# Kernel tuning notes

Hardware: AMD Instinct MI355X
Metric: run time of the kernel (lower is better)

## Reference

```python
import jax, jax.numpy as jnp
import numpy as np
from math import exp

C1 = 0.01 ** 2
C2 = 0.03 ** 2
WINDOW_SIZE = 11
SIGMA = 1.5

def make_window(window_size, channel, sigma=SIGMA):
    g = np.array([exp(-(x - window_size // 2) ** 2 / float(2 * sigma ** 2))
                  for x in range(window_size)], dtype=np.float32)
    g = g / g.sum()
    w2d = np.outer(g, g).astype(np.float32)  # [ws, ws]
    # depthwise kernel, OIHW with I=1 per group: [C, 1, ws, ws]
    return jnp.asarray(np.broadcast_to(w2d, (channel, 1, window_size, window_size)).copy())

def depthwise_conv(x, window, pad):
    C = x.shape[1]
    return jax.lax.conv_general_dilated(
        x, window, window_strides=(1, 1),
        padding=[(pad, pad), (pad, pad)],
        feature_group_count=C,
        dimension_numbers=('NCHW', 'OIHW', 'NCHW'))

def setup_inputs() -> dict:
    key = jax.random.key(0)
    k1, k2 = jax.random.split(key)
    B, C, H, W = 16, 3, 512, 512
    img1 = jax.random.uniform(k1, (B, C, H, W), dtype=jnp.float32)
    img2 = jax.random.uniform(k2, (B, C, H, W), dtype=jnp.float32)
    window = make_window(WINDOW_SIZE, C)
    return {"img1": img1, "img2": img2, "window": window}

def reference(img1, img2, window):
    pad = WINDOW_SIZE // 2
    mu1 = depthwise_conv(img1, window, pad)
    mu2 = depthwise_conv(img2, window, pad)
    mu1_sq = mu1 * mu1
    mu2_sq = mu2 * mu2
    mu1_mu2 = mu1 * mu2
    sigma1_sq = depthwise_conv(img1 * img1, window, pad) - mu1_sq
    sigma2_sq = depthwise_conv(img2 * img2, window, pad) - mu2_sq
    sigma12 = depthwise_conv(img1 * img2, window, pad) - mu1_mu2
    ssim_cs = (2 * sigma12 + C2) / (sigma1_sq + sigma2_sq + C2)
    ssim_l = (2 * mu1_mu2 + C1) / (mu1_sq + mu2_sq + C1)
    ssim_map = ssim_l * ssim_cs
    return jnp.mean(ssim_map)
```

## Files before the change

### kernel.cpp

```cpp
#include <hip/hip_runtime.h>


typedef float v2f __attribute__((ext_vector_type(2)));

#define IMG_H 512
#define IMG_W 512
#define N_IMG 48
#define WS 11
#define PAD 5
#define CHUNK 16
#define NCHUNK (IMG_H / CHUNK)
#define RING 12
#define PLANE_B 5248
#define NPLANE 4
#define INV_NPX (1.0f / (48.0f * 512.0f * 512.0f))

__device__ __forceinline__ unsigned swz8(int E) {
    return (unsigned)((E + (E >> 2)) * 8);
}
__device__ __forceinline__ v2f vfma(v2f a, v2f b, v2f c) {
    return __builtin_elementwise_fma(a, b, c);
}
__device__ __forceinline__ float uni(float x) {
    return __int_as_float(__builtin_amdgcn_readfirstlane(__float_as_int(x)));
}

__global__ __launch_bounds__(256, 5) void ssim_partial_kernel(
    const float* __restrict__ img1,
    const float* __restrict__ img2,
    const float* __restrict__ window,
    float* __restrict__ out)
{
    __shared__ __align__(16) char lds[NPLANE * PLANE_B];
    __shared__ float wred[4];

    const int tid = threadIdx.x;
    const int bc  = blockIdx.x;
    const int r0  = blockIdx.y * CHUNK;
    const int c0  = tid * 2;

    float g[WS];
    {
        const float g5  = sqrtf(window[5 * WS + 5]);
        const float inv = 1.0f / g5;
#pragma unroll
        for (int j = 0; j < WS; ++j) g[j] = uni(window[5 * WS + j] * inv);
    }
    const float C1v = 0.01f * 0.01f;
    const float C2v = 0.03f * 0.03f;

    const float* __restrict__ p1 = img1 + (size_t)bc * (IMG_H * IMG_W);
    const float* __restrict__ p2 = img2 + (size_t)bc * (IMG_H * IMG_W);

    if (tid < 48) {
        const int pj = tid / 12, h = tid % 12;
        const int E  = (h < 6) ? h : (512 + h);
        *(v2f*)(lds + pj * PLANE_B + swz8(E)) = (v2f)(0.0f);
    }
    __syncthreads();

    const unsigned woffA = swz8(c0 + 6);
    const unsigned woffB = swz8(c0 + 7);
    unsigned roff[12];
#pragma unroll
    for (int m = 0; m < 12; ++m) roff[m] = swz8(c0 + 1 + m);

    v2f rx1[RING], rx2[RING];
#pragma unroll
    for (int i = 0; i < RING; ++i) { rx1[i] = (v2f)(0.0f); rx2[i] = (v2f)(0.0f); }

#pragma unroll
    for (int i = 0; i < 10; ++i) {
        const int rr = r0 - PAD + i;
        v2f u1 = (v2f)(0.0f), u2 = (v2f)(0.0f);
        if (rr >= 0 && rr < IMG_H) {
            u1 = *(const v2f*)(p1 + rr * IMG_W + c0);
            u2 = *(const v2f*)(p2 + rr * IMG_W + c0);
        }
        rx1[2 + i] = u1; rx2[2 + i] = u2;
    }
    v2f pend1[2], pend2[2];
#pragma unroll
    for (int j = 0; j < 2; ++j) {
        const int rr = r0 + PAD + j;
        v2f u1 = (v2f)(0.0f), u2 = (v2f)(0.0f);
        if (rr < IMG_H) {
            u1 = *(const v2f*)(p1 + rr * IMG_W + c0);
            u2 = *(const v2f*)(p2 + rr * IMG_W + c0);
        }
        pend1[j] = u1; pend2[j] = u2;
    }

    float acc = 0.0f;

#pragma unroll 1
    for (int step = 0; step < CHUNK / 2; ++step) {
        const int R = r0 + step * 2;

#pragma unroll
        for (int i = 0; i < RING - 2; ++i) { rx1[i] = rx1[i + 2]; rx2[i] = rx2[i + 2]; }
        rx1[10] = pend1[0]; rx2[10] = pend2[0];
        rx1[11] = pend1[1]; rx2[11] = pend2[1];

        if (step + 1 < CHUNK / 2) {
#pragma unroll
            for (int j = 0; j < 2; ++j) {
                const int rr = R + 7 + j;
                v2f u1 = (v2f)(0.0f), u2 = (v2f)(0.0f);
                if (rr < IMG_H) {
                    u1 = *(const v2f*)(p1 + rr * IMG_W + c0);
                    u2 = *(const v2f*)(p2 + rr * IMG_W + c0);
                }
                pend1[j] = u1; pend2[j] = u2;
            }
        }

        v2f va[4][2];
        {
            v2f a0[2] = {(v2f)(0.0f), (v2f)(0.0f)};
            v2f a1[2] = {(v2f)(0.0f), (v2f)(0.0f)};
#pragma unroll
            for (int k = 0; k < 2; ++k)
#pragma unroll
                for (int i = 0; i < WS; ++i) {
                    const v2f w = (v2f)(g[i]);
                    a0[k] = vfma(w, rx1[i + k], a0[k]);
                    a1[k] = vfma(w, rx2[i + k], a1[k]);
                }
            va[0][0] = a0[0]; va[0][1] = a0[1];
            va[1][0] = a1[0]; va[1][1] = a1[1];
        }
        {
            v2f b0[2] = {(v2f)(0.0f), (v2f)(0.0f)};
            v2f b1[2] = {(v2f)(0.0f), (v2f)(0.0f)};
#pragma unroll
            for (int u = 0; u < RING; ++u) {
                const v2f X1 = rx1[u], X2 = rx2[u];
                const v2f S = vfma(X1, X1, X2 * X2);
                const v2f P = X1 * X2;
                if (u <= 10) {
                    b0[0] = vfma((v2f)(g[u]), S, b0[0]);
                    b1[0] = vfma((v2f)(g[u]), P, b1[0]);
                }
                if (u >= 1) {
                    b0[1] = vfma((v2f)(g[u - 1]), S, b0[1]);
                    b1[1] = vfma((v2f)(g[u - 1]), P, b1[1]);
                }
            }
            va[2][0] = b0[0]; va[2][1] = b0[1];
            va[3][0] = b1[0]; va[3][1] = b1[1];
        }
#pragma unroll
        for (int p = 0; p < 4; ++p) {
            char* base = lds + p * PLANE_B;
            *(v2f*)(base + woffA) = (v2f){va[p][0].x, va[p][1].x};
            *(v2f*)(base + woffB) = (v2f){va[p][0].y, va[p][1].y};
        }
        __syncthreads();

        v2f hA[4], hB[4];
#pragma unroll
        for (int p = 0; p < 4; ++p) {
            const char* base = lds + p * PLANE_B;
            v2f r[12];
#pragma unroll
            for (int m = 0; m < 12; ++m) r[m] = *(const v2f*)(base + roff[m]);
            v2f sA = (v2f)(0.0f), sB = (v2f)(0.0f);
#pragma unroll
            for (int i = 0; i < WS; ++i) {
                const v2f w = (v2f)(g[i]);
                sA = vfma(w, r[i],     sA);
                sB = vfma(w, r[i + 1], sB);
            }
            hA[p] = sA; hB[p] = sB;
        }
#pragma unroll
        for (int d = 0; d < 2; ++d) {
            const v2f mu1 = d ? hB[0] : hA[0];
            const v2f mu2 = d ? hB[1] : hA[1];
            const v2f hs  = d ? hB[2] : hA[2];
            const v2f hp  = d ? hB[3] : hA[3];
            const v2f mu1s = mu1 * mu1;
            const v2f mu2s = mu2 * mu2;
            const v2f mu12 = mu1 * mu2;
            const v2f sgs  = hs - mu1s - mu2s;
            const v2f sg12 = hp - mu12;
            const v2f num  = (2.f * mu12 + (v2f)(C1v)) * (2.f * sg12 + (v2f)(C2v));
            const v2f den  = (mu1s + mu2s + (v2f)(C1v)) * (sgs + (v2f)(C2v));
            v2f r = {__builtin_amdgcn_rcpf(den.x), __builtin_amdgcn_rcpf(den.y)};
            r = r * vfma(-den, r, (v2f)(2.0f));
            acc = fmaf(num.x, r.x, acc);
            acc = fmaf(num.y, r.y, acc);
        }
        __syncthreads();
    }

#pragma unroll
    for (int off = 32; off > 0; off >>= 1)
        acc += __shfl_down(acc, off);
    if ((tid & 63) == 0) wred[tid >> 6] = acc;
    __syncthreads();
    if (tid == 0) {
        const float s = (wred[0] + wred[1]) + (wred[2] + wred[3]);
        atomicAdd(out, s * INV_NPX);
    }
}

extern "C" void kernel_launch(void* const* d_in, const int* in_sizes, int n_in,
                              void* d_out, int out_size, void* d_ws, size_t ws_size,
                              hipStream_t stream) {
    const float* img1   = (const float*)d_in[0];
    const float* img2   = (const float*)d_in[1];
    const float* window = (const float*)d_in[2];
    float* out = (float*)d_out;

    hipMemsetAsync(out, 0, sizeof(float), stream);
    dim3 grid(N_IMG, NCHUNK);
    ssim_partial_kernel<<<grid, 256, 0, stream>>>(img1, img2, window, out);
}
```

Baseline: 158.8 us.

## Interleave four conv planes per column in LDS as float4 for horizontal pass

Switches the LDS layout from four separate planes (one float2 per column pair) to two row-regions that store all four quantities (mu1, mu2, sum of squares, product) for a column as one float4. Each thread now writes two 16-byte vectors per row and reads 12 float4 values per row for the horizontal pass, which cuts the number of LDS instructions and address computations. The launch bound is raised from 5 to 6 blocks per CU. In exchange, the SSIM epilogue is computed in scalar form and the padded swizzle layout uses 16-byte granules, which may change bank-conflict behaviour.

```diff
diff --git a/kernel.cpp b/kernel.cpp
--- a/kernel.cpp
+++ b/kernel.cpp
@@ -2,6 +2,7 @@
 
 
 typedef float v2f __attribute__((ext_vector_type(2)));
+typedef float v4f __attribute__((ext_vector_type(4)));
 
 #define IMG_H 512
 #define IMG_W 512
@@ -11,27 +12,29 @@
 #define CHUNK 16
 #define NCHUNK (IMG_H / CHUNK)
 #define RING 12
-#define PLANE_B 5248
-#define NPLANE 4
+#define REG_B 12608
 #define INV_NPX (1.0f / (48.0f * 512.0f * 512.0f))
 
-__device__ __forceinline__ unsigned swz8(int E) {
-    return (unsigned)((E + (E >> 2)) * 8);
-}
-__device__ __forceinline__ v2f vfma(v2f a, v2f b, v2f c) {
+__device__ __forceinline__ v2f vfma2(v2f a, v2f b, v2f c) {
+    return __builtin_elementwise_fma(a, b, c);
+}
+__device__ __forceinline__ v4f vfma4(v4f a, v4f b, v4f c) {
     return __builtin_elementwise_fma(a, b, c);
 }
 __device__ __forceinline__ float uni(float x) {
     return __int_as_float(__builtin_amdgcn_readfirstlane(__float_as_int(x)));
 }
-
-__global__ __launch_bounds__(256, 5) void ssim_partial_kernel(
+__device__ __forceinline__ unsigned swz16(int E) {
+    return (unsigned)((E + (E >> 1)) * 16);
+}
+
+__global__ __launch_bounds__(256, 6) void ssim_partial_kernel(
     const float* __restrict__ img1,
     const float* __restrict__ img2,
     const float* __restrict__ window,
     float* __restrict__ out)
 {
-    __shared__ __align__(16) char lds[NPLANE * PLANE_B];
+    __shared__ __align__(16) char lds[2 * REG_B];
     __shared__ float wred[4];
 
     const int tid = threadIdx.x;
@@ -52,18 +55,14 @@
     const float* __restrict__ p1 = img1 + (size_t)bc * (IMG_H * IMG_W);
     const float* __restrict__ p2 = img2 + (size_t)bc * (IMG_H * IMG_W);
 
-    if (tid < 48) {
-        const int pj = tid / 12, h = tid % 12;
+    if (tid < 24) {
+        const int rg = tid / 12, h = tid % 12;
         const int E  = (h < 6) ? h : (512 + h);
-        *(v2f*)(lds + pj * PLANE_B + swz8(E)) = (v2f)(0.0f);
+        *(v4f*)(lds + rg * REG_B + swz16(E)) = (v4f)(0.0f);
     }
     __syncthreads();
 
-    const unsigned woffA = swz8(c0 + 6);
-    const unsigned woffB = swz8(c0 + 7);
-    unsigned roff[12];
-#pragma unroll
-    for (int m = 0; m < 12; ++m) roff[m] = swz8(c0 + 1 + m);
+    char* lbase = lds + 48 * tid;
 
     v2f rx1[RING], rx2[RING];
 #pragma unroll
@@ -115,82 +114,66 @@
             }
         }
 
-        v2f va[4][2];
-        {
-            v2f a0[2] = {(v2f)(0.0f), (v2f)(0.0f)};
-            v2f a1[2] = {(v2f)(0.0f), (v2f)(0.0f)};
-#pragma unroll
-            for (int k = 0; k < 2; ++k)
-#pragma unroll
-                for (int i = 0; i < WS; ++i) {
-                    const v2f w = (v2f)(g[i]);
-                    a0[k] = vfma(w, rx1[i + k], a0[k]);
-                    a1[k] = vfma(w, rx2[i + k], a1[k]);
-                }
-            va[0][0] = a0[0]; va[0][1] = a0[1];
-            va[1][0] = a1[0]; va[1][1] = a1[1];
-        }
-        {
-            v2f b0[2] = {(v2f)(0.0f), (v2f)(0.0f)};
-            v2f b1[2] = {(v2f)(0.0f), (v2f)(0.0f)};
-#pragma unroll
-            for (int u = 0; u < RING; ++u) {
-                const v2f X1 = rx1[u], X2 = rx2[u];
-                const v2f S = vfma(X1, X1, X2 * X2);
-                const v2f P = X1 * X2;
-                if (u <= 10) {
-                    b0[0] = vfma((v2f)(g[u]), S, b0[0]);
-                    b1[0] = vfma((v2f)(g[u]), P, b1[0]);
-                }
-                if (u >= 1) {
-                    b0[1] = vfma((v2f)(g[u - 1]), S, b0[1]);
-                    b1[1] = vfma((v2f)(g[u - 1]), P, b1[1]);
-                }
-            }
-            va[2][0] = b0[0]; va[2][1] = b0[1];
-            va[3][0] = b1[0]; va[3][1] = b1[1];
-        }
-#pragma unroll
-        for (int p = 0; p < 4; ++p) {
-            char* base = lds + p * PLANE_B;
-            *(v2f*)(base + woffA) = (v2f){va[p][0].x, va[p][1].x};
-            *(v2f*)(base + woffB) = (v2f){va[p][0].y, va[p][1].y};
-        }
-        __syncthreads();
-
-        v2f hA[4], hB[4];
-#pragma unroll
-        for (int p = 0; p < 4; ++p) {
-            const char* base = lds + p * PLANE_B;
-            v2f r[12];
-#pragma unroll
-            for (int m = 0; m < 12; ++m) r[m] = *(const v2f*)(base + roff[m]);
-            v2f sA = (v2f)(0.0f), sB = (v2f)(0.0f);
+        v2f a0[2] = {(v2f)(0.0f), (v2f)(0.0f)};
+        v2f a1[2] = {(v2f)(0.0f), (v2f)(0.0f)};
+#pragma unroll
+        for (int k = 0; k < 2; ++k)
 #pragma unroll
             for (int i = 0; i < WS; ++i) {
                 const v2f w = (v2f)(g[i]);
-                sA = vfma(w, r[i],     sA);
-                sB = vfma(w, r[i + 1], sB);
-            }
-            hA[p] = sA; hB[p] = sB;
-        }
-#pragma unroll
-        for (int d = 0; d < 2; ++d) {
-            const v2f mu1 = d ? hB[0] : hA[0];
-            const v2f mu2 = d ? hB[1] : hA[1];
-            const v2f hs  = d ? hB[2] : hA[2];
-            const v2f hp  = d ? hB[3] : hA[3];
-            const v2f mu1s = mu1 * mu1;
-            const v2f mu2s = mu2 * mu2;
-            const v2f mu12 = mu1 * mu2;
-            const v2f sgs  = hs - mu1s - mu2s;
-            const v2f sg12 = hp - mu12;
-            const v2f num  = (2.f * mu12 + (v2f)(C1v)) * (2.f * sg12 + (v2f)(C2v));
-            const v2f den  = (mu1s + mu2s + (v2f)(C1v)) * (sgs + (v2f)(C2v));
-            v2f r = {__builtin_amdgcn_rcpf(den.x), __builtin_amdgcn_rcpf(den.y)};
-            r = r * vfma(-den, r, (v2f)(2.0f));
-            acc = fmaf(num.x, r.x, acc);
-            acc = fmaf(num.y, r.y, acc);
+                a0[k] = vfma2(w, rx1[i + k], a0[k]);
+                a1[k] = vfma2(w, rx2[i + k], a1[k]);
+            }
+        v2f b0[2] = {(v2f)(0.0f), (v2f)(0.0f)};
+        v2f b1[2] = {(v2f)(0.0f), (v2f)(0.0f)};
+#pragma unroll
+        for (int u = 0; u < RING; ++u) {
+            const v2f X1 = rx1[u], X2 = rx2[u];
+            const v2f S = vfma2(X1, X1, X2 * X2);
+            const v2f P = X1 * X2;
+            if (u <= 10) {
+                b0[0] = vfma2((v2f)(g[u]), S, b0[0]);
+                b1[0] = vfma2((v2f)(g[u]), P, b1[0]);
+            }
+            if (u >= 1) {
+                b0[1] = vfma2((v2f)(g[u - 1]), S, b0[1]);
+                b1[1] = vfma2((v2f)(g[u - 1]), P, b1[1]);
+            }
+        }
+#pragma unroll
+        for (int k = 0; k < 2; ++k) {
+            const v4f w0 = (v4f){a0[k].x, a1[k].x, b0[k].x, b1[k].x};
+            const v4f w1 = (v4f){a0[k].y, a1[k].y, b0[k].y, b1[k].y};
+            *(v4f*)(lbase + k * REG_B + 144) = w0;
+            *(v4f*)(lbase + k * REG_B + 160) = w1;
+        }
+        __syncthreads();
+
+#pragma unroll
+        for (int k = 0; k < 2; ++k) {
+            v4f hA = (v4f)(0.0f), hB = (v4f)(0.0f);
+#pragma unroll
+            for (int m = 0; m < 12; ++m) {
+                const int K = 1 + m;
+                const v4f t = *(const v4f*)(lbase + k * REG_B + 16 * (K + (K >> 1)));
+                if (m <= 10) hA = vfma4((v4f)(g[m]),     t, hA);
+                if (m >= 1)  hB = vfma4((v4f)(g[m - 1]), t, hB);
+            }
+#pragma unroll
+            for (int d = 0; d < 2; ++d) {
+                const v4f h = d ? hB : hA;
+                const float mu1 = h.x, mu2 = h.y;
+                const float mu1s = mu1 * mu1;
+                const float mu2s = mu2 * mu2;
+                const float mu12 = mu1 * mu2;
+                const float sgs  = h.z - mu1s - mu2s;
+                const float sg12 = h.w - mu12;
+                const float num  = (2.f * mu12 + C1v) * (2.f * sg12 + C2v);
+                const float den  = (mu1s + mu2s + C1v) * (sgs + C2v);
+                float r = __builtin_amdgcn_rcpf(den);
+                r = r * fmaf(-den, r, 2.0f);
+                acc = fmaf(num, r, acc);
+            }
         }
         __syncthreads();
     }
```

After: 141.2 us. 11.1% less time.
